# Performance work log

Hardware: AMD Instinct MI355X
Metric: run time of the kernel (lower is better)

Reference implementation:

```python
import jax, jax.numpy as jnp
import numpy as np

BN_EPS = 1e-3  # keras BatchNormalization default epsilon
NEG_INF = -1e30


def _masked_row_softmax(adjT):
    # tf.sparse.softmax semantics: softmax over NONZERO entries of each row;
    # implicit zeros stay exactly zero.
    mask = adjT != 0
    logits = jnp.where(mask, adjT, NEG_INF)
    p = jax.nn.softmax(logits, axis=-1)
    return jnp.where(mask, p, 0.0)


def _batch_norm(x, gamma, beta):
    # training-mode BN over all axes except channels
    mean = jnp.mean(x, axis=(0, 1), keepdims=True)
    var = jnp.var(x, axis=(0, 1), keepdims=True)
    return (x - mean) * jax.lax.rsqrt(var + BN_EPS) * gamma + beta


def setup_inputs() -> dict:
    key = jax.random.key(0)
    ks = jax.random.split(key, 4)
    B, N, F = 1, 8192, 128
    C0, C1 = 256, 128
    features = jax.random.normal(ks[0], (B, N, F), dtype=jnp.float32)
    adj = jax.random.randint(ks[1], (B, N, N), 0, 2, dtype=jnp.int32)
    kernel_1 = jax.random.normal(ks[2], (F, C0), dtype=jnp.float32) * (1.0 / np.sqrt(F))
    kernel_2 = jax.random.normal(ks[3], (C0, C1), dtype=jnp.float32) * (1.0 / np.sqrt(C0))
    return {
        "features": features,
        "adj": adj,
        "kernel_1": kernel_1,
        "bias_1": jnp.zeros((C0,), jnp.float32),
        "gamma_1": jnp.ones((C0,), jnp.float32),
        "beta_1": jnp.zeros((C0,), jnp.float32),
        "kernel_2": kernel_2,
        "bias_2": jnp.zeros((C1,), jnp.float32),
        "gamma_2": jnp.ones((C1,), jnp.float32),
        "beta_2": jnp.zeros((C1,), jnp.float32),
    }


def reference(features, adj, kernel_1, bias_1, gamma_1, beta_1,
              kernel_2, bias_2, gamma_2, beta_2):
    # fltr transposed: (B, Nr, Np), then sparse softmax over last dim
    adjT = jnp.transpose(adj.astype(jnp.float32), (0, 2, 1))
    w = _masked_row_softmax(adjT)                      # (B, Nr, Np)
    # people -> region aggregation + projection
    region = jnp.matmul(w, features)                   # (B, Nr, F)
    region = jnp.matmul(region, kernel_1) + bias_1     # (B, Nr, C0)
    region = _batch_norm(region, gamma_1, beta_1)
    # region -> people aggregation + projection
    people = jnp.matmul(jnp.transpose(w, (0, 2, 1)), region)  # (B, Np, C0)
    people = jnp.matmul(people, kernel_2) + bias_2             # (B, Np, C1)
    people = _batch_norm(people, gamma_2, beta_2)
    return people
```

## Files before the change

kernel.cpp:

```cpp
#include <hip/hip_runtime.h>
#include <stdint.h>

typedef unsigned int u32;
typedef unsigned short u16;
typedef unsigned long long u64;
typedef __attribute__((ext_vector_type(8))) short short8;
typedef __attribute__((ext_vector_type(4))) float f32x4;

#define N8K 8192

__device__ __forceinline__ float b2f(u16 u) { return __uint_as_float(((u32)u) << 16); }
__device__ __forceinline__ u16 f2b(float f) {
  u32 i = __float_as_uint(f);
  i += 0x7FFFu + ((i >> 16) & 1u);
  return (u16)(i >> 16);
}
__device__ __forceinline__ u32 pk01(int x, int y) { return (u32)__mul24(x | (y << 16), 0x3F80); }
__device__ __forceinline__ u32 pkf(float a, float b) { return (u32)f2b(a) | ((u32)f2b(b) << 16); }

__device__ __forceinline__ int dvote(const u16* f16) {
  u16 u = f16[threadIdx.x * 2];
  int e = (u >> 7) & 0xFF;
  return __syncthreads_count((e >= 0x60 && e <= 0x9F) ? 1 : 0) >= 128;
}

__device__ __forceinline__ void gl_lds16(const void* g, void* l) {
  __builtin_amdgcn_global_load_lds(
      (const __attribute__((address_space(1))) u32*)g,
      (__attribute__((address_space(3))) u32*)l, 16, 0, 0);
}

__device__ __forceinline__ void unpack16(u32 b, uint4& o0, uint4& o1) {
  o0.x = ((b & 0x0001u) ? 0x3F80u : 0u) | ((b & 0x0002u) ? 0x3F800000u : 0u);
  o0.y = ((b & 0x0004u) ? 0x3F80u : 0u) | ((b & 0x0008u) ? 0x3F800000u : 0u);
  o0.z = ((b & 0x0010u) ? 0x3F80u : 0u) | ((b & 0x0020u) ? 0x3F800000u : 0u);
  o0.w = ((b & 0x0040u) ? 0x3F80u : 0u) | ((b & 0x0080u) ? 0x3F800000u : 0u);
  o1.x = ((b & 0x0100u) ? 0x3F80u : 0u) | ((b & 0x0200u) ? 0x3F800000u : 0u);
  o1.y = ((b & 0x0400u) ? 0x3F80u : 0u) | ((b & 0x0800u) ? 0x3F800000u : 0u);
  o1.z = ((b & 0x1000u) ? 0x3F80u : 0u) | ((b & 0x2000u) ? 0x3F800000u : 0u);
  o1.w = ((b & 0x4000u) ? 0x3F80u : 0u) | ((b & 0x8000u) ? 0x3F800000u : 0u);
}

#define MFMA_4x4(As_, Bs_, aoff_, boff_)                                         \
  {                                                                              \
    short8 afr[4], bfr[4];                                                       \
    _Pragma("unroll") for (int i_ = 0; i_ < 4; ++i_)                             \
      afr[i_] = *(const short8*)(As_ + aoff_[i_]);                               \
    _Pragma("unroll") for (int j_ = 0; j_ < 4; ++j_)                             \
      bfr[j_] = *(const short8*)(Bs_ + boff_[j_]);                               \
    _Pragma("unroll") for (int i_ = 0; i_ < 4; ++i_)                             \
      _Pragma("unroll") for (int j_ = 0; j_ < 4; ++j_)                           \
        acc[i_][j_] = __builtin_amdgcn_mfma_f32_16x16x32_bf16(                   \
            afr[i_], bfr[j_], acc[i_][j_], 0, 0, 0);                             \
  }

#define ZERO_ACC()                                                               \
  f32x4 acc[4][4];                                                               \
  {                                                                              \
    const f32x4 fz = {0.f, 0.f, 0.f, 0.f};                                       \
    _Pragma("unroll") for (int i_ = 0; i_ < 4; ++i_)                             \
      _Pragma("unroll") for (int j_ = 0; j_ < 4; ++j_) acc[i_][j_] = fz;         \
  }

__global__ void k_prep(const void* __restrict__ featv, const void* __restrict__ K1v,
                       const void* __restrict__ K2v,
                       const void* __restrict__ b1v, const void* __restrict__ g1v,
                       const void* __restrict__ be1v, const void* __restrict__ b2v,
                       const void* __restrict__ g2v, const void* __restrict__ be2v,
                       u16* __restrict__ Ft, u16* __restrict__ K1T, u16* __restrict__ K2T,
                       float* __restrict__ deg, float* __restrict__ par,
                       float* __restrict__ bn1s, float* __restrict__ bn1q,
                       float* __restrict__ bn2s, float* __restrict__ bn2q) {
  const int b = blockIdx.x, t = threadIdx.x;
  const int flag = dvote((const u16*)featv);
  if (b < 256) {
    __shared__ __align__(16) u16 Lf[32 * 136];
    const int pr = t >> 3, ck = t & 7;
    u16 v[16];
    if (flag) {
      const u16* s = (const u16*)featv + (size_t)(b * 32 + pr) * 128 + ck * 16;
      *(uint4*)&v[0] = *(const uint4*)(s);
      *(uint4*)&v[8] = *(const uint4*)(s + 8);
    } else {
      const float* s = (const float*)featv + (size_t)(b * 32 + pr) * 128 + ck * 16;
#pragma unroll
      for (int i = 0; i < 16; ++i) v[i] = f2b(s[i]);
    }
    *(uint4*)(Lf + pr * 136 + ck * 16) = *(uint4*)&v[0];
    *(uint4*)(Lf + pr * 136 + ck * 16 + 8) = *(uint4*)&v[8];
    __syncthreads();
    const int f = t >> 1, h16 = (t & 1) * 16;
    u32 w[8];
#pragma unroll
    for (int i = 0; i < 8; ++i) {
      u16 lo = Lf[(h16 + 2 * i) * 136 + f];
      u16 hi = Lf[(h16 + 2 * i + 1) * 136 + f];
      w[i] = (u32)lo | ((u32)hi << 16);
    }
    u16* d = Ft + (size_t)b * 4096 + f * 32 + h16;
    *(uint4*)(d) = *(uint4*)&w[0];
    *(uint4*)(d + 8) = *(uint4*)&w[4];
  } else if (b < 272) {
    int o = ((b - 256) * 256 + t) << 3;
    int k0 = o >> 13, c = (o >> 5) & 255, kk = o & 31;
    uint4 w;
    if (flag) {
      const u16* s = (const u16*)K1v + (size_t)(k0 * 32 + kk) * 256 + c;
      w.x = (u32)s[0]    | ((u32)s[256]  << 16);
      w.y = (u32)s[512]  | ((u32)s[768]  << 16);
      w.z = (u32)s[1024] | ((u32)s[1280] << 16);
      w.w = (u32)s[1536] | ((u32)s[1792] << 16);
    } else {
      const float* s = (const float*)K1v + (size_t)(k0 * 32 + kk) * 256 + c;
      w.x = pkf(s[0], s[256]); w.y = pkf(s[512], s[768]);
      w.z = pkf(s[1024], s[1280]); w.w = pkf(s[1536], s[1792]);
    }
    *(uint4*)(K1T + o) = w;
  } else if (b < 288) {
    int o = ((b - 272) * 256 + t) << 3;
    int k0 = o >> 12, c = (o >> 5) & 127, kk = o & 31;
    uint4 w;
    if (flag) {
      const u16* s = (const u16*)K2v + (size_t)(k0 * 32 + kk) * 128 + c;
      w.x = (u32)s[0]   | ((u32)s[128] << 16);
      w.y = (u32)s[256] | ((u32)s[384] << 16);
      w.z = (u32)s[512] | ((u32)s[640] << 16);
      w.w = (u32)s[768] | ((u32)s[896] << 16);
    } else {
      const float* s = (const float*)K2v + (size_t)(k0 * 32 + kk) * 128 + c;
      w.x = pkf(s[0], s[128]); w.y = pkf(s[256], s[384]);
      w.z = pkf(s[512], s[640]); w.w = pkf(s[768], s[896]);
    }
    *(uint4*)(K2T + o) = w;
  } else {
    if (t < 256) {
      par[t]       = flag ? b2f(((const u16*)b1v)[t])  : ((const float*)b1v)[t];
      par[256 + t] = flag ? b2f(((const u16*)g1v)[t])  : ((const float*)g1v)[t];
      par[512 + t] = flag ? b2f(((const u16*)be1v)[t]) : ((const float*)be1v)[t];
      bn1s[t] = 0.f; bn1q[t] = 0.f;
    }
    if (t < 128) {
      par[768 + t]  = flag ? b2f(((const u16*)b2v)[t])  : ((const float*)b2v)[t];
      par[896 + t]  = flag ? b2f(((const u16*)g2v)[t])  : ((const float*)g2v)[t];
      par[1024 + t] = flag ? b2f(((const u16*)be2v)[t]) : ((const float*)be2v)[t];
      bn2s[t] = 0.f; bn2q[t] = 0.f;
    }
    for (int i = t; i < N8K; i += 256) deg[i] = 0.f;
  }
}

__global__ __launch_bounds__(256, 2)
void k_gemm1(const int* __restrict__ adj, const u16* __restrict__ Ft,
             float* __restrict__ P1, float* __restrict__ deg,
             u32* __restrict__ RB, int ksteps) {
  __shared__ __align__(16) u16 As[128 * 32];
  __shared__ __align__(16) u16 Bs[128 * 32];
  __shared__ float degp[128];
  const int t = threadIdx.x, bx = blockIdx.x;
  const int nt = bx & 63, s = bx >> 6;
  const int n0 = nt << 7;
  const int lane = t & 63, wv = t >> 6;
  const int wm = (wv & 1) << 6, wn = (wv >> 1) << 6;
  const int fm = lane & 15, fq = lane >> 4;
  if (t < 128) degp[t] = 0.0f;
  ZERO_ACC();
  int aoff[4], boff[4];
#pragma unroll
  for (int i = 0; i < 4; ++i) aoff[i] = (wm + i * 16 + fm) * 32 + fq * 8;
#pragma unroll
  for (int j = 0; j < 4; ++j) {
    int n = wn + j * 16 + fm;
    boff[j] = n * 32 + ((fq * 8) ^ (((n >> 2) & 3) << 3));
  }
  const int rb = t & 31, kb = t >> 5;
  const int* gB = adj + ((size_t)s * ksteps * 32 + kb * 4) * N8K + n0 + rb * 4;
  const char* gA = (const char*)(Ft + (size_t)s * ksteps * 4096);
  char* lA = (char*)As + ((t >> 6) << 10);
  const int goff = t << 4;
  u16* lb = Bs + (rb * 4) * 32 + ((kb * 4) ^ ((rb & 3) << 3));
  const int sh4 = (rb & 7) * 4;
  const int rbw = (n0 >> 5) + (rb >> 3);
  const int pb0 = s * ksteps * 32 + kb * 4;
  int ds0 = 0, ds1 = 0, ds2 = 0, ds3 = 0;
  for (int ks = 0; ks < ksteps; ++ks) {
    __syncthreads();
    gl_lds16(gA + goff, lA);
    gl_lds16(gA + 4096 + goff, lA + 4096);
    int4 a0 = *(const int4*)(gB);
    int4 a1 = *(const int4*)(gB + N8K);
    int4 a2 = *(const int4*)(gB + 2 * N8K);
    int4 a3 = *(const int4*)(gB + 3 * N8K);
    gA += 8192;
    gB += 32 * N8K;
    ds0 += a0.x + a1.x + a2.x + a3.x;
    ds1 += a0.y + a1.y + a2.y + a3.y;
    ds2 += a0.z + a1.z + a2.z + a3.z;
    ds3 += a0.w + a1.w + a2.w + a3.w;
    uint2 w;
    w.x = pk01(a0.x, a1.x); w.y = pk01(a2.x, a3.x); *(uint2*)(lb) = w;
    w.x = pk01(a0.y, a1.y); w.y = pk01(a2.y, a3.y); *(uint2*)(lb + 32) = w;
    w.x = pk01(a0.z, a1.z); w.y = pk01(a2.z, a3.z); *(uint2*)(lb + 64) = w;
    w.x = pk01(a0.w, a1.w); w.y = pk01(a2.w, a3.w); *(uint2*)(lb + 96) = w;
    u32 v0 = ((u32)a0.x | ((u32)a0.y << 1) | ((u32)a0.z << 2) | ((u32)a0.w << 3)) << sh4;
    u32 v1 = ((u32)a1.x | ((u32)a1.y << 1) | ((u32)a1.z << 2) | ((u32)a1.w << 3)) << sh4;
    u32 v2 = ((u32)a2.x | ((u32)a2.y << 1) | ((u32)a2.z << 2) | ((u32)a2.w << 3)) << sh4;
    u32 v3 = ((u32)a3.x | ((u32)a3.y << 1) | ((u32)a3.z << 2) | ((u32)a3.w << 3)) << sh4;
    v0 |= __shfl_xor(v0, 1); v0 |= __shfl_xor(v0, 2); v0 |= __shfl_xor(v0, 4);
    v1 |= __shfl_xor(v1, 1); v1 |= __shfl_xor(v1, 2); v1 |= __shfl_xor(v1, 4);
    v2 |= __shfl_xor(v2, 1); v2 |= __shfl_xor(v2, 2); v2 |= __shfl_xor(v2, 4);
    v3 |= __shfl_xor(v3, 1); v3 |= __shfl_xor(v3, 2); v3 |= __shfl_xor(v3, 4);
    if ((rb & 7) == 0) {
      u32* dst = RB + (size_t)(pb0 + ks * 32) * 256 + rbw;
      dst[0] = v0; dst[256] = v1; dst[512] = v2; dst[768] = v3;
    }
    __syncthreads();
    MFMA_4x4(As, Bs, aoff, boff);
  }
  atomicAdd(&degp[rb * 4 + 0], (float)ds0);
  atomicAdd(&degp[rb * 4 + 1], (float)ds1);
  atomicAdd(&degp[rb * 4 + 2], (float)ds2);
  atomicAdd(&degp[rb * 4 + 3], (float)ds3);
  float* base = P1 + ((size_t)s * N8K + n0) * 128;
#pragma unroll
  for (int i = 0; i < 4; ++i)
#pragma unroll
    for (int j = 0; j < 4; ++j) {
      int r = wn + j * 16 + fm;
      int f = wm + i * 16 + fq * 4;
      *(f32x4*)(base + (size_t)r * 128 + f) = acc[i][j];
    }
  __syncthreads();
  if (t < 128) atomicAdd(&deg[n0 + t], degp[t]);
}

__global__ __launch_bounds__(256, 2)
void k_projf(const float* __restrict__ Psrc, const float* __restrict__ deg,
             const u16* __restrict__ Bt, const float* __restrict__ bias,
             float* __restrict__ Cout, float* __restrict__ bns, float* __restrict__ bnq,
             int nsplit, int ksteps, int Ncols, int useinv) {
  __shared__ __align__(16) u16 As[128 * 32];
  __shared__ __align__(16) u16 Bs[128 * 32];
  const int t = threadIdx.x, bx = blockIdx.x;
  const int ct = bx & 1, mt = (bx >> 1) & 63;
  const int m0 = mt << 7, n0 = ct << 7;
  const int lane = t & 63, wv = t >> 6;
  const int wm = (wv & 1) << 6, wn = (wv >> 1) << 6;
  const int fm = lane & 15, fq = lane >> 4;
  const int K = ksteps << 5;
  ZERO_ACC();
  int aoff[4], boff[4];
#pragma unroll
  for (int i = 0; i < 4; ++i) {
    int m = wm + i * 16 + fm;
    aoff[i] = m * 32 + ((fq * 8) ^ (((m >> 2) & 3) << 3));
  }
#pragma unroll
  for (int j = 0; j < 4; ++j) boff[j] = (wn + j * 16 + fm) * 32 + fq * 8;
  const int row = t >> 1;
  const size_t sstride = (size_t)N8K * K;
  const float* src = Psrc + (size_t)(m0 + row) * K + (t & 1) * 16;
  float inv = 1.0f;
  if (useinv) {
    float d = deg[m0 + row];
    inv = (d > 0.5f) ? 1.0f / d : 0.0f;
  }
  const int swzA = ((t >> 3) & 3) << 3;
  u16* la0 = As + row * 32 + (((t & 1) * 16) ^ swzA);
  u16* la1 = As + row * 32 + ((((t & 1) * 16) + 8) ^ swzA);
  char* lB = (char*)Bs + ((t >> 6) << 10);
  const int goff = t << 4;
  for (int ks = 0; ks < ksteps; ++ks) {
    __syncthreads();
    const char* gB = (const char*)(Bt + ((size_t)ks * Ncols + n0) * 32);
    gl_lds16(gB + goff, lB);
    gl_lds16(gB + 4096 + goff, lB + 4096);
    f32x4 s0 = {0.f, 0.f, 0.f, 0.f}, s1 = s0, s2 = s0, s3 = s0;
    const float* p = src + ks * 32;
    for (int sp = 0; sp < nsplit; ++sp) {
      const f32x4* q = (const f32x4*)(p + sp * sstride);
      s0 += q[0]; s1 += q[1]; s2 += q[2]; s3 += q[3];
    }
    s0 *= inv; s1 *= inv; s2 *= inv; s3 *= inv;
    uint4 w;
    w.x = pkf(s0[0], s0[1]); w.y = pkf(s0[2], s0[3]);
    w.z = pkf(s1[0], s1[1]); w.w = pkf(s1[2], s1[3]);
    *(uint4*)la0 = w;
    w.x = pkf(s2[0], s2[1]); w.y = pkf(s2[2], s2[3]);
    w.z = pkf(s3[0], s3[1]); w.w = pkf(s3[2], s3[3]);
    *(uint4*)la1 = w;
    __syncthreads();
    MFMA_4x4(As, Bs, aoff, boff);
  }
#pragma unroll
  for (int j = 0; j < 4; ++j) {
    int c = n0 + wn + j * 16 + fm;
    float bc = bias[c];
    float t1 = 0.f, t2 = 0.f;
#pragma unroll
    for (int i = 0; i < 4; ++i) {
      int r = m0 + wm + i * 16 + fq * 4;
#pragma unroll
      for (int ii = 0; ii < 4; ++ii) {
        float v = acc[i][j][ii] + bc;
        Cout[(size_t)(r + ii) * Ncols + c] = v;
        t1 += v; t2 += v * v;
      }
    }
    t1 += __shfl_xor(t1, 16); t1 += __shfl_xor(t1, 32);
    t2 += __shfl_xor(t2, 16); t2 += __shfl_xor(t2, 32);
    if (fq == 0) { atomicAdd(&bns[c], t1); atomicAdd(&bnq[c], t2); }
  }
}

__global__ __launch_bounds__(256, 2)
void k_bnH(const float* __restrict__ region1, const float* __restrict__ deg,
           const float* __restrict__ bn1s, const float* __restrict__ bn1q,
           const float* __restrict__ g1, const float* __restrict__ be1,
           const u16* __restrict__ K2T, u16* __restrict__ HT) {
  __shared__ __align__(16) u16 As[128 * 32];
  __shared__ __align__(16) u16 Bs[128 * 32];
  __shared__ float scS[256], shS[256];
  const int t = threadIdx.x, mt = blockIdx.x;
  const int m0 = mt << 7;
  const int lane = t & 63, wv = t >> 6;
  const int wm = (wv & 1) << 6, wn = (wv >> 1) << 6;
  const int fm = lane & 15, fq = lane >> 4;
  {
    float mu = bn1s[t] * (1.0f / 8192.0f);
    float var = bn1q[t] * (1.0f / 8192.0f) - mu * mu;
    float iv = rsqrtf(var + 1e-3f);
    float sc = iv * g1[t];
    scS[t] = sc;
    shS[t] = be1[t] - mu * sc;
  }
  ZERO_ACC();
  int aoff[4], boff[4];
#pragma unroll
  for (int i = 0; i < 4; ++i) {
    int m = wm + i * 16 + fm;
    aoff[i] = m * 32 + ((fq * 8) ^ (((m >> 2) & 3) << 3));
  }
#pragma unroll
  for (int j = 0; j < 4; ++j) boff[j] = (wn + j * 16 + fm) * 32 + fq * 8;
  const int row = t >> 1, half = t & 1;
  float d = deg[m0 + row];
  const float idg = (d > 0.5f) ? 1.0f / d : 0.0f;
  const float* src = region1 + (size_t)(m0 + row) * 256 + half * 16;
  const int swzA = ((t >> 3) & 3) << 3;
  u16* la0 = As + row * 32 + ((half * 16) ^ swzA);
  u16* la1 = As + row * 32 + (((half * 16) + 8) ^ swzA);
  char* lB = (char*)Bs + ((t >> 6) << 10);
  const int goff = t << 4;
  for (int ks = 0; ks < 8; ++ks) {
    __syncthreads();
    const char* gB = (const char*)(K2T + (size_t)ks * 4096);
    gl_lds16(gB + goff, lB);
    gl_lds16(gB + 4096 + goff, lB + 4096);
    const float* p = src + ks * 32;
    const int cb = ks * 32 + half * 16;
    float y[16];
#pragma unroll
    for (int q = 0; q < 4; ++q) {
      f32x4 x = *(const f32x4*)(p + q * 4);
#pragma unroll
      for (int jj = 0; jj < 4; ++jj)
        y[q * 4 + jj] = (x[jj] * scS[cb + q * 4 + jj] + shS[cb + q * 4 + jj]) * idg;
    }
    uint4 w;
    w.x = pkf(y[0], y[1]); w.y = pkf(y[2], y[3]);
    w.z = pkf(y[4], y[5]); w.w = pkf(y[6], y[7]);
    *(uint4*)la0 = w;
    w.x = pkf(y[8], y[9]); w.y = pkf(y[10], y[11]);
    w.z = pkf(y[12], y[13]); w.w = pkf(y[14], y[15]);
    *(uint4*)la1 = w;
    __syncthreads();
    MFMA_4x4(As, Bs, aoff, boff);
  }
#pragma unroll
  for (int i = 0; i < 4; ++i)
#pragma unroll
    for (int j = 0; j < 4; ++j) {
      int c = wn + j * 16 + fm;
      int r = m0 + wm + i * 16 + fq * 4;
      uint2 w;
      w.x = pkf(acc[i][j][0], acc[i][j][1]);
      w.y = pkf(acc[i][j][2], acc[i][j][3]);
      *(uint2*)(HT + (size_t)(r >> 5) * 4096 + c * 32 + (r & 31)) = w;
    }
}

__global__ __launch_bounds__(256, 2)
void k_gemm2(const u32* __restrict__ RB, const u16* __restrict__ HT,
             float* __restrict__ P2, int ksteps) {
  __shared__ __align__(16) u16 As[128 * 32];
  __shared__ __align__(16) u16 Bs[128 * 32];
  const int t = threadIdx.x, bx = blockIdx.x;
  const int mt = bx & 63, s = bx >> 6;
  const int m0 = mt << 7;
  const int lane = t & 63, wv = t >> 6;
  const int wm = (wv & 1) << 6, wn = (wv >> 1) << 6;
  const int fm = lane & 15, fq = lane >> 4;
  ZERO_ACC();
  int aoff[4], boff[4];
#pragma unroll
  for (int i = 0; i < 4; ++i) {
    int m = wm + i * 16 + fm;
    aoff[i] = m * 32 + ((fq * 8) ^ (((m >> 2) & 3) << 3));
  }
#pragma unroll
  for (int j = 0; j < 4; ++j) boff[j] = (wn + j * 16 + fm) * 32 + fq * 8;
  const int row = t >> 1, h = t & 1;
  const u32* gA = RB + (size_t)(m0 + row) * 256 + s * ksteps;
  const char* gB = (const char*)(HT + (size_t)s * ksteps * 4096);
  char* lB = (char*)Bs + ((t >> 6) << 10);
  const int goff = t << 4;
  const int swzA = ((row >> 2) & 3) << 3;
  u16* la0 = As + row * 32 + ((h * 16) ^ swzA);
  u16* la1 = As + row * 32 + (((h * 16) + 8) ^ swzA);
  for (int ks = 0; ks < ksteps; ++ks) {
    __syncthreads();
    gl_lds16(gB + goff, lB);
    gl_lds16(gB + 4096 + goff, lB + 4096);
    u32 w = gA[ks];
    gB += 8192;
    u32 bits = (w >> (h * 16)) & 0xFFFFu;
    uint4 o0, o1;
    unpack16(bits, o0, o1);
    *(uint4*)la0 = o0;
    *(uint4*)la1 = o1;
    __syncthreads();
    MFMA_4x4(As, Bs, aoff, boff);
  }
  float* base = P2 + (size_t)s * N8K * 128;
#pragma unroll
  for (int i = 0; i < 4; ++i)
#pragma unroll
    for (int j = 0; j < 4; ++j) {
      int c = wn + j * 16 + fm;
      int pr = m0 + wm + i * 16 + fq * 4;
#pragma unroll
      for (int ii = 0; ii < 4; ++ii)
        base[(size_t)(pr + ii) * 128 + c] = acc[i][j][ii];
    }
}

__global__ void k_red2(const float* __restrict__ P2, const float* __restrict__ bias,
                       float* __restrict__ people1,
                       float* __restrict__ bn2s, float* __restrict__ bn2q) {
  __shared__ float r1[256], r2[256];
  const int t = threadIdx.x;
  const int c = t & 127, pg = t >> 7;
  const int p0 = blockIdx.x << 5;
  const float bc = bias[c];
  float s1 = 0.f, s2 = 0.f;
  for (int pp = pg; pp < 32; pp += 2) {
    size_t o = (size_t)(p0 + pp) * 128 + c;
    float v = bc;
#pragma unroll
    for (int s = 0; s < 8; ++s) v += P2[(size_t)s * N8K * 128 + o];
    people1[o] = v;
    s1 += v; s2 += v * v;
  }
  r1[t] = s1; r2[t] = s2;
  __syncthreads();
  if (t < 128) {
    atomicAdd(&bn2s[t], r1[t] + r1[t + 128]);
    atomicAdd(&bn2q[t], r2[t] + r2[t + 128]);
  }
}

__global__ void k_bn2apply(const float* __restrict__ people1,
                           const float* __restrict__ bn2s, const float* __restrict__ bn2q,
                           const float* __restrict__ g2, const float* __restrict__ be2,
                           const u16* __restrict__ featprobe, void* __restrict__ outv) {
  const int flag = dvote(featprobe);
  int g = blockIdx.x * 256 + threadIdx.x;
  int p = g >> 5;
  int c = (g & 31) << 2;
  f32x4 x = *(const f32x4*)(people1 + (size_t)p * 128 + c);
  f32x4 y;
#pragma unroll
  for (int jj = 0; jj < 4; ++jj) {
    int cc = c + jj;
    float mu = bn2s[cc] * (1.0f / 8192.0f);
    float var = bn2q[cc] * (1.0f / 8192.0f) - mu * mu;
    float inv = rsqrtf(var + 1e-3f);
    y[jj] = (x[jj] - mu) * inv * g2[cc] + be2[cc];
  }
  if (flag) {
    uint2 w;
    w.x = pkf(y[0], y[1]);
    w.y = pkf(y[2], y[3]);
    *(uint2*)((u16*)outv + (size_t)p * 128 + c) = w;
  } else {
    *(f32x4*)((float*)outv + (size_t)p * 128 + c) = y;
  }
}

extern "C" void kernel_launch(void* const* d_in, const int* in_sizes, int n_in,
                              void* d_out, int out_size, void* d_ws, size_t ws_size,
                              hipStream_t stream) {
  const void* feat = d_in[0];
  const int* adj   = (const int*)d_in[1];
  const void* K1   = d_in[2];
  const void* b1   = d_in[3];
  const void* g1   = d_in[4];
  const void* be1  = d_in[5];
  const void* K2   = d_in[6];
  const void* b2   = d_in[7];
  const void* g2   = d_in[8];
  const void* be2  = d_in[9];
  char* ws = (char*)d_ws;
  const size_t MB = 1u << 20;

  float* Pbig    = (float*)(ws);
  float* region1 = (float*)(ws + 32 * MB);
  float* people1 = (float*)(ws + 40 * MB);
  u16*   Ft      = (u16*)(ws + 44 * MB);
  u16*   HT      = (u16*)(ws + 46 * MB);
  u32*   RB      = (u32*)(ws + 48 * MB);
  u16*   K1T     = (u16*)(ws + 56 * MB);
  u16*   K2T     = K1T + 32768;
  float* deg     = (float*)(K2T + 32768);
  float* par     = deg + N8K;
  float* bn1s    = par + 1152;
  float* bn1q    = bn1s + 256;
  float* bn2s    = bn1q + 256;
  float* bn2q    = bn2s + 128;

  k_prep<<<289, 256, 0, stream>>>(feat, K1, K2, b1, g1, be1, b2, g2, be2,
                                  Ft, K1T, K2T, deg, par, bn1s, bn1q, bn2s, bn2q);
  k_gemm1<<<512, 256, 0, stream>>>(adj, Ft, Pbig, deg, RB, 32);
  k_projf<<<128, 256, 0, stream>>>(Pbig, deg, K1T, par + 0, region1, bn1s, bn1q,
                                   8, 4, 256, 1);
  k_bnH<<<64, 256, 0, stream>>>(region1, deg, bn1s, bn1q, par + 256, par + 512,
                                K2T, HT);
  k_gemm2<<<512, 256, 0, stream>>>(RB, HT, Pbig, 32);
  k_red2<<<256, 256, 0, stream>>>(Pbig, par + 768, people1, bn2s, bn2q);
  k_bn2apply<<<1024, 256, 0, stream>>>(people1, bn2s, bn2q, par + 896, par + 1024,
                                       (const u16*)feat, d_out);
}
```

Before: 480.8 us.

## Double K-depth per iteration in big GEMMs and shrink tiles in small projection kernels

In k_gemm1 and k_gemm2 each loop iteration now stages two 32-wide K slices into doubled LDS buffers and issues two MFMA tile passes, which halves the iteration count and the number of barriers per K range. The adjacency loads for both slices are issued together, so more global memory traffic is in flight per iteration. k_projf uses 64-row tiles and k_bnH uses 32-row tiles with smaller per-wave accumulator sets, raising their block counts from 128 and 64 to 256 each to fill more CUs. The cost is double the LDS per block in the big GEMMs, which can lower occupancy, and more register pressure from the extra loads held at once.

```diff
diff --git a/kernel.cpp b/kernel.cpp
--- a/kernel.cpp
+++ b/kernel.cpp
@@ -152,9 +152,9 @@
 __global__ __launch_bounds__(256, 2)
 void k_gemm1(const int* __restrict__ adj, const u16* __restrict__ Ft,
              float* __restrict__ P1, float* __restrict__ deg,
-             u32* __restrict__ RB, int ksteps) {
-  __shared__ __align__(16) u16 As[128 * 32];
-  __shared__ __align__(16) u16 Bs[128 * 32];
+             u32* __restrict__ RB) {
+  __shared__ __align__(16) u16 As[2 * 128 * 32];
+  __shared__ __align__(16) u16 Bs[2 * 128 * 32];
   __shared__ float degp[128];
   const int t = threadIdx.x, bx = blockIdx.x;
   const int nt = bx & 63, s = bx >> 6;
@@ -173,48 +173,69 @@
     boff[j] = n * 32 + ((fq * 8) ^ (((n >> 2) & 3) << 3));
   }
   const int rb = t & 31, kb = t >> 5;
-  const int* gB = adj + ((size_t)s * ksteps * 32 + kb * 4) * N8K + n0 + rb * 4;
-  const char* gA = (const char*)(Ft + (size_t)s * ksteps * 4096);
+  const int* gB = adj + ((size_t)s * 1024 + kb * 4) * N8K + n0 + rb * 4;
+  const char* gA = (const char*)(Ft + (size_t)s * 32 * 4096);
   char* lA = (char*)As + ((t >> 6) << 10);
   const int goff = t << 4;
-  u16* lb = Bs + (rb * 4) * 32 + ((kb * 4) ^ ((rb & 3) << 3));
+  u16* lb0 = Bs + (rb * 4) * 32 + ((kb * 4) ^ ((rb & 3) << 3));
+  u16* lb1 = lb0 + 4096;
   const int sh4 = (rb & 7) * 4;
   const int rbw = (n0 >> 5) + (rb >> 3);
-  const int pb0 = s * ksteps * 32 + kb * 4;
+  const int pb0 = s * 1024 + kb * 4;
   int ds0 = 0, ds1 = 0, ds2 = 0, ds3 = 0;
-  for (int ks = 0; ks < ksteps; ++ks) {
+  for (int ks = 0; ks < 16; ++ks) {
     __syncthreads();
     gl_lds16(gA + goff, lA);
     gl_lds16(gA + 4096 + goff, lA + 4096);
+    gl_lds16(gA + 8192 + goff, lA + 8192);
+    gl_lds16(gA + 12288 + goff, lA + 12288);
     int4 a0 = *(const int4*)(gB);
     int4 a1 = *(const int4*)(gB + N8K);
     int4 a2 = *(const int4*)(gB + 2 * N8K);
     int4 a3 = *(const int4*)(gB + 3 * N8K);
-    gA += 8192;
-    gB += 32 * N8K;
-    ds0 += a0.x + a1.x + a2.x + a3.x;
-    ds1 += a0.y + a1.y + a2.y + a3.y;
-    ds2 += a0.z + a1.z + a2.z + a3.z;
-    ds3 += a0.w + a1.w + a2.w + a3.w;
+    int4 b0 = *(const int4*)(gB + 32 * N8K);
+    int4 b1 = *(const int4*)(gB + 33 * N8K);
+    int4 b2 = *(const int4*)(gB + 34 * N8K);
+    int4 b3 = *(const int4*)(gB + 35 * N8K);
+    gA += 16384;
+    gB += 64 * N8K;
+    ds0 += a0.x + a1.x + a2.x + a3.x + b0.x + b1.x + b2.x + b3.x;
+    ds1 += a0.y + a1.y + a2.y + a3.y + b0.y + b1.y + b2.y + b3.y;
+    ds2 += a0.z + a1.z + a2.z + a3.z + b0.z + b1.z + b2.z + b3.z;
+    ds3 += a0.w + a1.w + a2.w + a3.w + b0.w + b1.w + b2.w + b3.w;
     uint2 w;
-    w.x = pk01(a0.x, a1.x); w.y = pk01(a2.x, a3.x); *(uint2*)(lb) = w;
-    w.x = pk01(a0.y, a1.y); w.y = pk01(a2.y, a3.y); *(uint2*)(lb + 32) = w;
-    w.x = pk01(a0.z, a1.z); w.y = pk01(a2.z, a3.z); *(uint2*)(lb + 64) = w;
-    w.x = pk01(a0.w, a1.w); w.y = pk01(a2.w, a3.w); *(uint2*)(lb + 96) = w;
+    w.x = pk01(a0.x, a1.x); w.y = pk01(a2.x, a3.x); *(uint2*)(lb0) = w;
+    w.x = pk01(a0.y, a1.y); w.y = pk01(a2.y, a3.y); *(uint2*)(lb0 + 32) = w;
+    w.x = pk01(a0.z, a1.z); w.y = pk01(a2.z, a3.z); *(uint2*)(lb0 + 64) = w;
+    w.x = pk01(a0.w, a1.w); w.y = pk01(a2.w, a3.w); *(uint2*)(lb0 + 96) = w;
+    w.x = pk01(b0.x, b1.x); w.y = pk01(b2.x, b3.x); *(uint2*)(lb1) = w;
+    w.x = pk01(b0.y, b1.y); w.y = pk01(b2.y, b3.y); *(uint2*)(lb1 + 32) = w;
+    w.x = pk01(b0.z, b1.z); w.y = pk01(b2.z, b3.z); *(uint2*)(lb1 + 64) = w;
+    w.x = pk01(b0.w, b1.w); w.y = pk01(b2.w, b3.w); *(uint2*)(lb1 + 96) = w;
     u32 v0 = ((u32)a0.x | ((u32)a0.y << 1) | ((u32)a0.z << 2) | ((u32)a0.w << 3)) << sh4;
     u32 v1 = ((u32)a1.x | ((u32)a1.y << 1) | ((u32)a1.z << 2) | ((u32)a1.w << 3)) << sh4;
     u32 v2 = ((u32)a2.x | ((u32)a2.y << 1) | ((u32)a2.z << 2) | ((u32)a2.w << 3)) << sh4;
     u32 v3 = ((u32)a3.x | ((u32)a3.y << 1) | ((u32)a3.z << 2) | ((u32)a3.w << 3)) << sh4;
+    u32 v4 = ((u32)b0.x | ((u32)b0.y << 1) | ((u32)b0.z << 2) | ((u32)b0.w << 3)) << sh4;
+    u32 v5 = ((u32)b1.x | ((u32)b1.y << 1) | ((u32)b1.z << 2) | ((u32)b1.w << 3)) << sh4;
+    u32 v6 = ((u32)b2.x | ((u32)b2.y << 1) | ((u32)b2.z << 2) | ((u32)b2.w << 3)) << sh4;
+    u32 v7 = ((u32)b3.x | ((u32)b3.y << 1) | ((u32)b3.z << 2) | ((u32)b3.w << 3)) << sh4;
     v0 |= __shfl_xor(v0, 1); v0 |= __shfl_xor(v0, 2); v0 |= __shfl_xor(v0, 4);
     v1 |= __shfl_xor(v1, 1); v1 |= __shfl_xor(v1, 2); v1 |= __shfl_xor(v1, 4);
     v2 |= __shfl_xor(v2, 1); v2 |= __shfl_xor(v2, 2); v2 |= __shfl_xor(v2, 4);
     v3 |= __shfl_xor(v3, 1); v3 |= __shfl_xor(v3, 2); v3 |= __shfl_xor(v3, 4);
+    v4 |= __shfl_xor(v4, 1); v4 |= __shfl_xor(v4, 2); v4 |= __shfl_xor(v4, 4);
+    v5 |= __shfl_xor(v5, 1); v5 |= __shfl_xor(v5, 2); v5 |= __shfl_xor(v5, 4);
+    v6 |= __shfl_xor(v6, 1); v6 |= __shfl_xor(v6, 2); v6 |= __shfl_xor(v6, 4);
+    v7 |= __shfl_xor(v7, 1); v7 |= __shfl_xor(v7, 2); v7 |= __shfl_xor(v7, 4);
     if ((rb & 7) == 0) {
-      u32* dst = RB + (size_t)(pb0 + ks * 32) * 256 + rbw;
+      u32* dst = RB + (size_t)(pb0 + ks * 64) * 256 + rbw;
       dst[0] = v0; dst[256] = v1; dst[512] = v2; dst[768] = v3;
+      dst[8192] = v4; dst[8448] = v5; dst[8704] = v6; dst[8960] = v7;
     }
     __syncthreads();
     MFMA_4x4(As, Bs, aoff, boff);
+    MFMA_4x4((As + 4096), (Bs + 4096), aoff, boff);
   }
   atomicAdd(&degp[rb * 4 + 0], (float)ds0);
   atomicAdd(&degp[rb * 4 + 1], (float)ds1);
@@ -234,75 +255,80 @@
 }
 
 __global__ __launch_bounds__(256, 2)
-void k_projf(const float* __restrict__ Psrc, const float* __restrict__ deg,
-             const u16* __restrict__ Bt, const float* __restrict__ bias,
-             float* __restrict__ Cout, float* __restrict__ bns, float* __restrict__ bnq,
-             int nsplit, int ksteps, int Ncols, int useinv) {
-  __shared__ __align__(16) u16 As[128 * 32];
+void k_projf(const float* __restrict__ P1, const float* __restrict__ deg,
+             const u16* __restrict__ K1T, const float* __restrict__ bias,
+             float* __restrict__ Cout, float* __restrict__ bns, float* __restrict__ bnq) {
+  __shared__ __align__(16) u16 As[64 * 32];
   __shared__ __align__(16) u16 Bs[128 * 32];
   const int t = threadIdx.x, bx = blockIdx.x;
-  const int ct = bx & 1, mt = (bx >> 1) & 63;
-  const int m0 = mt << 7, n0 = ct << 7;
+  const int ct = bx & 1, mt = bx >> 1;
+  const int m0 = mt << 6, n0 = ct << 7;
   const int lane = t & 63, wv = t >> 6;
-  const int wm = (wv & 1) << 6, wn = (wv >> 1) << 6;
+  const int wn = wv << 5;
   const int fm = lane & 15, fq = lane >> 4;
-  const int K = ksteps << 5;
-  ZERO_ACC();
-  int aoff[4], boff[4];
+  const f32x4 fz = {0.f, 0.f, 0.f, 0.f};
+  f32x4 acc[4][2];
+#pragma unroll
+  for (int i = 0; i < 4; ++i)
+#pragma unroll
+    for (int j = 0; j < 2; ++j) acc[i][j] = fz;
+  int aoff[4], boff[2];
 #pragma unroll
   for (int i = 0; i < 4; ++i) {
-    int m = wm + i * 16 + fm;
+    int m = i * 16 + fm;
     aoff[i] = m * 32 + ((fq * 8) ^ (((m >> 2) & 3) << 3));
   }
 #pragma unroll
-  for (int j = 0; j < 4; ++j) boff[j] = (wn + j * 16 + fm) * 32 + fq * 8;
-  const int row = t >> 1;
-  const size_t sstride = (size_t)N8K * K;
-  const float* src = Psrc + (size_t)(m0 + row) * K + (t & 1) * 16;
-  float inv = 1.0f;
-  if (useinv) {
-    float d = deg[m0 + row];
-    inv = (d > 0.5f) ? 1.0f / d : 0.0f;
-  }
-  const int swzA = ((t >> 3) & 3) << 3;
-  u16* la0 = As + row * 32 + (((t & 1) * 16) ^ swzA);
-  u16* la1 = As + row * 32 + ((((t & 1) * 16) + 8) ^ swzA);
+  for (int j = 0; j < 2; ++j) boff[j] = (wn + j * 16 + fm) * 32 + fq * 8;
+  const int row = t >> 2, q = t & 3;
+  const float* src = P1 + (size_t)(m0 + row) * 128 + q * 8;
+  float d = deg[m0 + row];
+  const float inv = (d > 0.5f) ? 1.0f / d : 0.0f;
+  const int swz = ((row >> 2) & 3) << 3;
+  u16* la = As + row * 32 + ((q * 8) ^ swz);
   char* lB = (char*)Bs + ((t >> 6) << 10);
   const int goff = t << 4;
-  for (int ks = 0; ks < ksteps; ++ks) {
-    __syncthreads();
-    const char* gB = (const char*)(Bt + ((size_t)ks * Ncols + n0) * 32);
+  for (int ks = 0; ks < 4; ++ks) {
+    __syncthreads();
+    const char* gB = (const char*)(K1T + ((size_t)ks * 256 + n0) * 32);
     gl_lds16(gB + goff, lB);
     gl_lds16(gB + 4096 + goff, lB + 4096);
-    f32x4 s0 = {0.f, 0.f, 0.f, 0.f}, s1 = s0, s2 = s0, s3 = s0;
+    f32x4 s0 = fz, s1 = fz;
     const float* p = src + ks * 32;
-    for (int sp = 0; sp < nsplit; ++sp) {
-      const f32x4* q = (const f32x4*)(p + sp * sstride);
-      s0 += q[0]; s1 += q[1]; s2 += q[2]; s3 += q[3];
-    }
-    s0 *= inv; s1 *= inv; s2 *= inv; s3 *= inv;
+#pragma unroll
+    for (int sp = 0; sp < 8; ++sp) {
+      const f32x4* q4 = (const f32x4*)(p + (size_t)sp * N8K * 128);
+      s0 += q4[0]; s1 += q4[1];
+    }
+    s0 *= inv; s1 *= inv;
     uint4 w;
     w.x = pkf(s0[0], s0[1]); w.y = pkf(s0[2], s0[3]);
     w.z = pkf(s1[0], s1[1]); w.w = pkf(s1[2], s1[3]);
-    *(uint4*)la0 = w;
-    w.x = pkf(s2[0], s2[1]); w.y = pkf(s2[2], s2[3]);
-    w.z = pkf(s3[0], s3[1]); w.w = pkf(s3[2], s3[3]);
-    *(uint4*)la1 = w;
-    __syncthreads();
-    MFMA_4x4(As, Bs, aoff, boff);
-  }
-#pragma unroll
-  for (int j = 0; j < 4; ++j) {
+    *(uint4*)la = w;
+    __syncthreads();
+    short8 afr[4], bfr[2];
+#pragma unroll
+    for (int i = 0; i < 4; ++i) afr[i] = *(const short8*)(As + aoff[i]);
+#pragma unroll
+    for (int j = 0; j < 2; ++j) bfr[j] = *(const short8*)(Bs + boff[j]);
+#pragma unroll
+    for (int i = 0; i < 4; ++i)
+#pragma unroll
+      for (int j = 0; j < 2; ++j)
+        acc[i][j] = __builtin_amdgcn_mfma_f32_16x16x32_bf16(afr[i], bfr[j], acc[i][j], 0, 0, 0);
+  }
+#pragma unroll
+  for (int j = 0; j < 2; ++j) {
     int c = n0 + wn + j * 16 + fm;
     float bc = bias[c];
     float t1 = 0.f, t2 = 0.f;
 #pragma unroll
     for (int i = 0; i < 4; ++i) {
-      int r = m0 + wm + i * 16 + fq * 4;
+      int r = m0 + i * 16 + fq * 4;
 #pragma unroll
       for (int ii = 0; ii < 4; ++ii) {
         float v = acc[i][j][ii] + bc;
-        Cout[(size_t)(r + ii) * Ncols + c] = v;
+        Cout[(size_t)(r + ii) * 256 + c] = v;
         t1 += v; t2 += v * v;
       }
     }
@@ -317,13 +343,13 @@
            const float* __restrict__ bn1s, const float* __restrict__ bn1q,
            const float* __restrict__ g1, const float* __restrict__ be1,
            const u16* __restrict__ K2T, u16* __restrict__ HT) {
-  __shared__ __align__(16) u16 As[128 * 32];
+  __shared__ __align__(16) u16 As[32 * 32];
   __shared__ __align__(16) u16 Bs[128 * 32];
   __shared__ float scS[256], shS[256];
   const int t = threadIdx.x, mt = blockIdx.x;
-  const int m0 = mt << 7;
+  const int m0 = mt << 5;
   const int lane = t & 63, wv = t >> 6;
-  const int wm = (wv & 1) << 6, wn = (wv >> 1) << 6;
+  const int wn = wv << 5;
   const int fm = lane & 15, fq = lane >> 4;
   {
     float mu = bn1s[t] * (1.0f / 8192.0f);
@@ -333,22 +359,26 @@
     scS[t] = sc;
     shS[t] = be1[t] - mu * sc;
   }
-  ZERO_ACC();
-  int aoff[4], boff[4];
-#pragma unroll
-  for (int i = 0; i < 4; ++i) {
-    int m = wm + i * 16 + fm;
+  const f32x4 fz = {0.f, 0.f, 0.f, 0.f};
+  f32x4 acc[2][2];
+#pragma unroll
+  for (int i = 0; i < 2; ++i)
+#pragma unroll
+    for (int j = 0; j < 2; ++j) acc[i][j] = fz;
+  int aoff[2], boff[2];
+#pragma unroll
+  for (int i = 0; i < 2; ++i) {
+    int m = i * 16 + fm;
     aoff[i] = m * 32 + ((fq * 8) ^ (((m >> 2) & 3) << 3));
   }
 #pragma unroll
-  for (int j = 0; j < 4; ++j) boff[j] = (wn + j * 16 + fm) * 32 + fq * 8;
-  const int row = t >> 1, half = t & 1;
+  for (int j = 0; j < 2; ++j) boff[j] = (wn + j * 16 + fm) * 32 + fq * 8;
+  const int row = t >> 3, oct = t & 7;
   float d = deg[m0 + row];
   const float idg = (d > 0.5f) ? 1.0f / d : 0.0f;
-  const float* src = region1 + (size_t)(m0 + row) * 256 + half * 16;
-  const int swzA = ((t >> 3) & 3) << 3;
-  u16* la0 = As + row * 32 + ((half * 16) ^ swzA);
-  u16* la1 = As + row * 32 + (((half * 16) + 8) ^ swzA);
+  const float* src = region1 + (size_t)(m0 + row) * 256 + oct * 4;
+  const int swz = ((row >> 2) & 3) << 3;
+  u16* la = As + row * 32 + ((oct * 4) ^ swz);
   char* lB = (char*)Bs + ((t >> 6) << 10);
   const int goff = t << 4;
   for (int ks = 0; ks < 8; ++ks) {
@@ -356,32 +386,33 @@
     const char* gB = (const char*)(K2T + (size_t)ks * 4096);
     gl_lds16(gB + goff, lB);
     gl_lds16(gB + 4096 + goff, lB + 4096);
-    const float* p = src + ks * 32;
-    const int cb = ks * 32 + half * 16;
-    float y[16];
-#pragma unroll
-    for (int q = 0; q < 4; ++q) {
-      f32x4 x = *(const f32x4*)(p + q * 4);
-#pragma unroll
-      for (int jj = 0; jj < 4; ++jj)
-        y[q * 4 + jj] = (x[jj] * scS[cb + q * 4 + jj] + shS[cb + q * 4 + jj]) * idg;
-    }
-    uint4 w;
-    w.x = pkf(y[0], y[1]); w.y = pkf(y[2], y[3]);
-    w.z = pkf(y[4], y[5]); w.w = pkf(y[6], y[7]);
-    *(uint4*)la0 = w;
-    w.x = pkf(y[8], y[9]); w.y = pkf(y[10], y[11]);
-    w.z = pkf(y[12], y[13]); w.w = pkf(y[14], y[15]);
-    *(uint4*)la1 = w;
-    __syncthreads();
-    MFMA_4x4(As, Bs, aoff, boff);
-  }
-#pragma unroll
-  for (int i = 0; i < 4; ++i)
-#pragma unroll
-    for (int j = 0; j < 4; ++j) {
+    const int cb = ks * 32 + oct * 4;
+    f32x4 x = *(const f32x4*)(src + ks * 32);
+    float y[4];
+#pragma unroll
+    for (int jj = 0; jj < 4; ++jj) y[jj] = (x[jj] * scS[cb + jj] + shS[cb + jj]) * idg;
+    uint2 w;
+    w.x = pkf(y[0], y[1]);
+    w.y = pkf(y[2], y[3]);
+    *(uint2*)la = w;
+    __syncthreads();
+    short8 afr[2], bfr[2];
+#pragma unroll
+    for (int i = 0; i < 2; ++i) afr[i] = *(const short8*)(As + aoff[i]);
+#pragma unroll
+    for (int j = 0; j < 2; ++j) bfr[j] = *(const short8*)(Bs + boff[j]);
+#pragma unroll
+    for (int i = 0; i < 2; ++i)
+#pragma unroll
+      for (int j = 0; j < 2; ++j)
+        acc[i][j] = __builtin_amdgcn_mfma_f32_16x16x32_bf16(afr[i], bfr[j], acc[i][j], 0, 0, 0);
+  }
+#pragma unroll
+  for (int i = 0; i < 2; ++i)
+#pragma unroll
+    for (int j = 0; j < 2; ++j) {
       int c = wn + j * 16 + fm;
-      int r = m0 + wm + i * 16 + fq * 4;
+      int r = m0 + i * 16 + fq * 4;
       uint2 w;
       w.x = pkf(acc[i][j][0], acc[i][j][1]);
       w.y = pkf(acc[i][j][2], acc[i][j][3]);
@@ -391,9 +422,9 @@
 
 __global__ __launch_bounds__(256, 2)
 void k_gemm2(const u32* __restrict__ RB, const u16* __restrict__ HT,
-             float* __restrict__ P2, int ksteps) {
-  __shared__ __align__(16) u16 As[128 * 32];
-  __shared__ __align__(16) u16 Bs[128 * 32];
+             float* __restrict__ P2) {
+  __shared__ __align__(16) u16 As[2 * 128 * 32];
+  __shared__ __align__(16) u16 Bs[2 * 128 * 32];
   const int t = threadIdx.x, bx = blockIdx.x;
   const int mt = bx & 63, s = bx >> 6;
   const int m0 = mt << 7;
@@ -410,26 +441,33 @@
 #pragma unroll
   for (int j = 0; j < 4; ++j) boff[j] = (wn + j * 16 + fm) * 32 + fq * 8;
   const int row = t >> 1, h = t & 1;
-  const u32* gA = RB + (size_t)(m0 + row) * 256 + s * ksteps;
-  const char* gB = (const char*)(HT + (size_t)s * ksteps * 4096);
+  const u32* gA = RB + (size_t)(m0 + row) * 256 + s * 32;
+  const char* gB = (const char*)(HT + (size_t)s * 32 * 4096);
   char* lB = (char*)Bs + ((t >> 6) << 10);
   const int goff = t << 4;
   const int swzA = ((row >> 2) & 3) << 3;
   u16* la0 = As + row * 32 + ((h * 16) ^ swzA);
   u16* la1 = As + row * 32 + (((h * 16) + 8) ^ swzA);
-  for (int ks = 0; ks < ksteps; ++ks) {
+  for (int ks = 0; ks < 16; ++ks) {
     __syncthreads();
     gl_lds16(gB + goff, lB);
     gl_lds16(gB + 4096 + goff, lB + 4096);
-    u32 w = gA[ks];
-    gB += 8192;
-    u32 bits = (w >> (h * 16)) & 0xFFFFu;
+    gl_lds16(gB + 8192 + goff, lB + 8192);
+    gl_lds16(gB + 12288 + goff, lB + 12288);
+    uint2 w2 = *(const uint2*)(gA + ks * 2);
+    gB += 16384;
+    u32 bits0 = (w2.x >> (h * 16)) & 0xFFFFu;
+    u32 bits1 = (w2.y >> (h * 16)) & 0xFFFFu;
     uint4 o0, o1;
-    unpack16(bits, o0, o1);
+    unpack16(bits0, o0, o1);
     *(uint4*)la0 = o0;
     *(uint4*)la1 = o1;
+    unpack16(bits1, o0, o1);
+    *(uint4*)(la0 + 4096) = o0;
+    *(uint4*)(la1 + 4096) = o1;
     __syncthreads();
     MFMA_4x4(As, Bs, aoff, boff);
+    MFMA_4x4((As + 4096), (Bs + 4096), aoff, boff);
   }
   float* base = P2 + (size_t)s * N8K * 128;
 #pragma unroll
@@ -530,12 +568,11 @@
 
   k_prep<<<289, 256, 0, stream>>>(feat, K1, K2, b1, g1, be1, b2, g2, be2,
                                   Ft, K1T, K2T, deg, par, bn1s, bn1q, bn2s, bn2q);
-  k_gemm1<<<512, 256, 0, stream>>>(adj, Ft, Pbig, deg, RB, 32);
-  k_projf<<<128, 256, 0, stream>>>(Pbig, deg, K1T, par + 0, region1, bn1s, bn1q,
-                                   8, 4, 256, 1);
-  k_bnH<<<64, 256, 0, stream>>>(region1, deg, bn1s, bn1q, par + 256, par + 512,
-                                K2T, HT);
-  k_gemm2<<<512, 256, 0, stream>>>(RB, HT, Pbig, 32);
+  k_gemm1<<<512, 256, 0, stream>>>(adj, Ft, Pbig, deg, RB);
+  k_projf<<<256, 256, 0, stream>>>(Pbig, deg, K1T, par + 0, region1, bn1s, bn1q);
+  k_bnH<<<256, 256, 0, stream>>>(region1, deg, bn1s, bn1q, par + 256, par + 512,
+                                 K2T, HT);
+  k_gemm2<<<512, 256, 0, stream>>>(RB, HT, Pbig);
   k_red2<<<256, 256, 0, stream>>>(Pbig, par + 768, people1, bn2s, bn2q);
   k_bn2apply<<<1024, 256, 0, stream>>>(people1, bn2s, bn2q, par + 896, par + 1024,
                                        (const u16*)feat, d_out);
```

After: 466.1 us. 1.03x faster.
